# Kernel optimization log

Hardware: AMD Instinct MI355X
Metric: run time of the kernel (lower is better)

## Reference

```python
import jax, jax.numpy as jnp
from jax import lax
import numpy as np

S, D, H, DW, V, KW = 2048, 512, 512, 512, 100000, 3


def _build_gaz(rng):
    lens = rng.integers(2, 9, size=(S, KW))
    keep = (rng.random((S, KW)) < 0.5) & (np.arange(S)[:, None] + lens - 1 < S)
    word_ids = rng.integers(0, V, size=(S, KW))
    ends = [[] for _ in range(S)]
    for s in range(S):
        for j in range(KW):
            if keep[s, j]:
                ends[s + lens[s, j] - 1].append((s, j))
    Km = max(1, max(len(e) for e in ends))
    gpos = np.zeros((S, Km), np.int32)
    gslot = np.zeros((S, Km), np.int32)
    gmask = np.zeros((S, Km), bool)
    for t in range(S):
        for k, (s, j) in enumerate(ends[t]):
            gpos[t, k], gslot[t, k], gmask[t, k] = s, j, True
    return word_ids.astype(np.int32), gpos, gslot, gmask


def setup_inputs() -> dict:
    rng = np.random.default_rng(0)
    word_ids, gpos, gslot, gmask = _build_gaz(rng)
    key = jax.random.key(0)
    ks = jax.random.split(key, 12)
    f32 = jnp.float32
    inp = {
        "x": jax.random.normal(ks[0], (1, S, D), f32),
        # MultiInputLSTMCell params
        "W_ih": jax.random.normal(ks[1], (D, 3 * H), f32) / np.sqrt(D),
        "W_hh": jax.random.normal(ks[2], (H, 3 * H), f32) / np.sqrt(H),
        "b": jnp.zeros((3 * H,), f32),
        "aW_ih": jax.random.normal(ks[3], (D, H), f32) / np.sqrt(D),
        "aW_hh": jax.random.normal(ks[4], (H, H), f32) / np.sqrt(H),
        "ab": jnp.zeros((H,), f32),
        # WordLSTMCell params
        "Ww_ih": jax.random.normal(ks[5], (DW, 3 * H), f32) / np.sqrt(DW),
        "Ww_hh": jax.random.normal(ks[6], (H, 3 * H), f32) / np.sqrt(H),
        "bw": jnp.zeros((3 * H,), f32),
        # gaz word embedding table (dropout=0.0 -> identity)
        "word_emb": jax.random.normal(ks[7], (V, DW), f32) * 0.1,
        "word_ids": jnp.asarray(word_ids),
        "gather_pos": jnp.asarray(gpos),
        "gather_slot": jnp.asarray(gslot),
        "gather_mask": jnp.asarray(gmask),
    }
    return inp


def reference(x, W_ih, W_hh, b, aW_ih, aW_hh, ab, Ww_ih, Ww_hh, bw, word_emb,
              word_ids, gather_pos, gather_slot, gather_mask):
    xs = x[0]                                   # [S, D]
    WI = xs @ W_ih                              # [S, 3H] char-cell input proj
    AWI = xs @ aW_ih + ab                       # [S, H]  alpha input proj
    wemb = word_emb[word_ids]                   # [S, KW, DW] gaz embedding gather
    WWI = jnp.einsum('skd,dh->skh', wemb, Ww_ih)  # [S, KW, 3H] word-cell input proj
    gmaskf = gather_mask.astype(x.dtype)        # [S, Km]
    Hh = W_hh.shape[0]
    c_buf0 = jnp.zeros((S, word_ids.shape[1], Hh), x.dtype)  # word c^w storage by (start, slot)
    h0 = jnp.zeros((Hh,), x.dtype)
    c0 = jnp.zeros((Hh,), x.dtype)

    def step(carry, t):
        hx, cx, c_buf = carry
        # words ending at t (scattered earlier): [Km, H]
        c_in = c_buf[gather_pos[t], gather_slot[t]]
        m = gmaskf[t][:, None]
        # char cell gates
        gates = hx @ W_hh + b + WI[t]           # [3H]
        i, o, g = jnp.split(gates, 3)
        i = jax.nn.sigmoid(i); o = jax.nn.sigmoid(o); g = jnp.tanh(g)
        # exp-normalized blend over {char gate i} U {alpha_k} (masked)
        alpha = jax.nn.sigmoid(AWI[t][None, :] + c_in @ aW_hh)  # [Km, H]
        w_i = jnp.exp(i)                        # [H]
        w_a = jnp.exp(alpha) * m                # [Km, H]
        denom = w_i + w_a.sum(0)
        c_merge = (w_i * g + (w_a * c_in).sum(0)) / denom
        c_plain = (1.0 - i) * cx + i * g        # no-word branch: f = 1 - i
        has_words = gather_mask[t].any()
        c1 = jnp.where(has_words, c_merge, c_plain)
        h1 = o * jnp.tanh(c1)
        # word cells for words STARTING at t, seeded with updated (h1, c1)
        wgates = WWI[t] + (h1 @ Ww_hh + bw)[None, :]  # [KW, 3H]
        f, iw, gw = jnp.split(wgates, 3, axis=1)
        ct_w = jax.nn.sigmoid(f) * c1[None, :] + jax.nn.sigmoid(iw) * jnp.tanh(gw)
        c_buf = lax.dynamic_update_slice(c_buf, ct_w[None], (t, 0, 0))
        return (h1, c1, c_buf), (h1, c1)

    _, (hs, cs) = lax.scan(step, (h0, c0, c_buf0), jnp.arange(S))
    return hs[None], cs[None]                   # each [1, S, H]
```

## Files before the change

### kernel.cpp

```cpp
#include <hip/hip_runtime.h>

constexpr int SEQ = 2048;
constexpr int HD  = 512;
constexpr int TH3 = 1536;
constexpr int ZT  = 3072;
constexpr int KWW = 3;

constexpr int GRID = 64;
constexpr int NT   = 512;
constexpr int HB   = HD / GRID;
constexpr int SPB  = SEQ / GRID;
constexpr int MAXW = 16;

constexpr unsigned int SENT = 0xFFFFFFFFu;

constexpr size_t WS_FLAGS  = 0;
constexpr size_t WS_CNT    = 1024;
constexpr size_t WS_ZEROSZ = 2048;
constexpr size_t WS_CBUF   = 2048;
constexpr size_t WS_HFULL  = WS_CBUF + (size_t)SEQ*KWW*HD*4;
constexpr size_t WS_FFEND  = WS_HFULL + (size_t)SEQ*HD*4;
constexpr size_t WS_MHDR   = ((WS_FFEND + 255)/256)*256;
constexpr size_t WS_MROWS  = WS_MHDR + (size_t)SEQ*4;
constexpr size_t WS_WIB    = WS_MROWS + (size_t)SEQ*MAXW*4;
constexpr size_t WS_AWIB   = WS_WIB  + (size_t)SEQ*TH3*4;
constexpr size_t WS_WWIB   = WS_AWIB + (size_t)SEQ*HD*4;
constexpr size_t WS_WT     = WS_WWIB + (size_t)SEQ*KWW*TH3*4;
constexpr size_t WS_END    = WS_WT + (size_t)ZT*HD*4;

__device__ inline float bf2f(unsigned int u) {
    return __builtin_bit_cast(float, u << 16);
}
__device__ inline unsigned short f2bf(float f) {
    unsigned int u = __builtin_bit_cast(unsigned int, f);
    u += 0x7fffu + ((u >> 16) & 1u);
    return (unsigned short)(u >> 16);
}
__device__ inline float sigf(float x) { return 1.0f / (1.0f + expf(-x)); }

template <typename T>
__device__ inline T ldg_a(const T* p) {
    return __hip_atomic_load((T*)p, __ATOMIC_RELAXED, __HIP_MEMORY_SCOPE_AGENT);
}
template <typename T>
__device__ inline void stg_a(T* p, T v) {
    __hip_atomic_store(p, v, __ATOMIC_RELAXED, __HIP_MEMORY_SCOPE_AGENT);
}
__device__ inline unsigned int ldu_a(const unsigned int* p) {
    return __hip_atomic_load((unsigned int*)p, __ATOMIC_RELAXED, __HIP_MEMORY_SCOPE_AGENT);
}

__device__ inline float4 ld4e(const void* p, size_t eoff, int mode) {
    if (mode) {
        uint2 v = *(const uint2*)((const unsigned short*)p + eoff);
        return make_float4(bf2f(v.x & 0xffffu), bf2f(v.x >> 16),
                           bf2f(v.y & 0xffffu), bf2f(v.y >> 16));
    }
    return *(const float4*)((const float*)p + eoff);
}
__device__ inline float ld1e(const void* p, size_t eoff, int mode) {
    return mode ? bf2f((unsigned int)((const unsigned short*)p)[eoff])
                : ((const float*)p)[eoff];
}

constexpr int NDET = 4096;
__global__ void detect_kernel(const unsigned int* __restrict__ w, int* __restrict__ cnt) {
    int local = 0;
    for (int i = threadIdx.x; i < NDET; i += 256) {
        unsigned int e = (w[i] >> 7) & 0xffu;
        if (e >= 90u && e <= 140u) local++;
    }
    atomicAdd(cnt, local);
}

template<bool GATHER>
__global__ __launch_bounds__(256) void gemm_bias_kernel(
    const void* __restrict__ A, const void* __restrict__ B,
    const void* __restrict__ bias, const int* __restrict__ ids,
    const int* __restrict__ cnt,
    float* __restrict__ C, int M, int N, int K)
{
    const int mode = (*cnt > NDET / 2) ? 1 : 0;
    __shared__ __align__(16) float As[16][68];
    __shared__ __align__(16) float Bs[16][68];
    const int tid = threadIdx.x;
    const int ty = tid >> 4, tx = tid & 15;
    const int m0 = blockIdx.y * 64, n0 = blockIdx.x * 64;
    const int lrow = tid >> 2;
    const int kq   = (tid & 3) * 4;
    const int arow = m0 + lrow;
    const size_t abase = (GATHER ? (size_t)ids[arow] : (size_t)arow) * (size_t)K;
    const int brow = tid >> 4;
    const int bc   = (tid & 15) * 4;
    const int bcol = n0 + bc;
    float acc[4][4] = {};
    for (int k0 = 0; k0 < K; k0 += 16) {
        float4 av = ld4e(A, abase + k0 + kq, mode);
        float4 bv = ld4e(B, (size_t)(k0 + brow) * N + bcol, mode);
        As[kq + 0][lrow] = av.x;
        As[kq + 1][lrow] = av.y;
        As[kq + 2][lrow] = av.z;
        As[kq + 3][lrow] = av.w;
        Bs[brow][bc + 0] = bv.x;
        Bs[brow][bc + 1] = bv.y;
        Bs[brow][bc + 2] = bv.z;
        Bs[brow][bc + 3] = bv.w;
        __syncthreads();
        #pragma unroll
        for (int kk = 0; kk < 16; ++kk) {
            float a[4], bb[4];
            #pragma unroll
            for (int u = 0; u < 4; ++u) a[u] = As[kk][ty * 4 + u];
            #pragma unroll
            for (int v = 0; v < 4; ++v) bb[v] = Bs[kk][tx * 4 + v];
            #pragma unroll
            for (int u = 0; u < 4; ++u)
                #pragma unroll
                for (int v = 0; v < 4; ++v)
                    acc[u][v] = fmaf(a[u], bb[v], acc[u][v]);
        }
        __syncthreads();
    }
    float4 bsv = ld4e(bias, (size_t)(n0 + tx * 4), mode);
    #pragma unroll
    for (int u = 0; u < 4; ++u) {
        float4 o;
        o.x = acc[u][0] + bsv.x; o.y = acc[u][1] + bsv.y;
        o.z = acc[u][2] + bsv.z; o.w = acc[u][3] + bsv.w;
        *(float4*)(C + (size_t)(m0 + ty * 4 + u) * N + n0 + tx * 4) = o;
    }
}

__global__ __launch_bounds__(256) void transpose_cat_kernel(
    const void* __restrict__ W_hh, const void* __restrict__ Ww_hh,
    const int* __restrict__ cnt, float* __restrict__ out)
{
    const int mode = (*cnt > NDET / 2) ? 1 : 0;
    __shared__ float tile[32][33];
    const int c0 = blockIdx.x * 32;
    const int j0 = blockIdx.y * 32;
    const int tx = threadIdx.x & 31, ty = threadIdx.x >> 5;
    const void* src = (c0 < TH3) ? W_hh : Ww_hh;
    const int cc0 = (c0 < TH3) ? c0 : c0 - TH3;
    #pragma unroll
    for (int dy = 0; dy < 32; dy += 8)
        tile[ty + dy][tx] = ld1e(src, (size_t)(j0 + ty + dy) * TH3 + cc0 + tx, mode);
    __syncthreads();
    #pragma unroll
    for (int dy = 0; dy < 32; dy += 8)
        out[(size_t)(c0 + ty + dy) * HD + j0 + tx] = tile[tx][ty + dy];
}

__device__ inline void gbar(int* flags, int b, int k) {
    __atomic_signal_fence(__ATOMIC_SEQ_CST);
    __builtin_amdgcn_s_waitcnt(0);
    __syncthreads();
    if (threadIdx.x < 64) {
        if (threadIdx.x == 0) stg_a(&flags[b], k);
        for (;;) {
            int v = ldg_a(&flags[threadIdx.x]);
            if (__all(v >= k)) break;
            __builtin_amdgcn_s_sleep(1);
        }
    }
    __syncthreads();
    __atomic_signal_fence(__ATOMIC_SEQ_CST);
}

__device__ inline float wave_red(float acc) {
    #pragma unroll
    for (int m = 1; m < 64; m <<= 1) acc += __shfl_xor(acc, m, 64);
    return acc;
}

__global__ __launch_bounds__(NT, 1) void lattice_scan(
    const float* WT, const void* __restrict__ aW_hh,
    const float* __restrict__ WIb, const float* __restrict__ AWIb,
    const float* __restrict__ WWIb,
    float* hfull, float* c_buf, int* __restrict__ flags,
    const int* __restrict__ cnt,
    const int* __restrict__ gpos, const int* __restrict__ gslot,
    const unsigned char* __restrict__ gmaskb,
    int* __restrict__ meta_hdr, int* __restrict__ meta_rows,
    void* __restrict__ outp, int Km)
{
    __shared__ __align__(16) float cinS[2][MAXW][HD];
    __shared__ int mh_l[2], mr_l[2][MAXW];
    __shared__ int mfmt;

    const int b    = blockIdx.x;
    const int tid  = threadIdx.x;
    const int wid  = tid >> 6;
    const int q    = tid & 63;
    const int mode = (*cnt > NDET / 2) ? 1 : 0;
    const int hb0  = b * HB;
    const int ch   = hb0 + wid;

    float wreg[6][8];
    #pragma unroll
    for (int k = 0; k < 6; ++k)
        #pragma unroll
        for (int i = 0; i < 8; ++i)
            wreg[k][i] = WT[(size_t)(k * HD + ch) * HD + q + 64 * i];
    float aw[8];
    #pragma unroll
    for (int i = 0; i < 8; ++i)
        aw[i] = ld1e(aW_hh, (size_t)(q + 64 * i) * HD + ch, mode);

    if (tid == 0) mfmt = 0;
    __syncthreads();
    {
        int any = 0;
        int tot = SEQ * Km;
        for (int i = tid; i < tot; i += NT)
            if ((i & 3) && gmaskb[i]) any = 1;
        if (any) mfmt = 1;
    }
    __syncthreads();
    const int maskfmt = mfmt;
    const int* gmi = (const int*)gmaskb;

    if (tid < SPB) {
        int t = b * SPB + tid;
        int nv = 0;
        for (int k = 0; k < Km; ++k) {
            int mv = maskfmt ? (int)gmaskb[t * Km + k] : gmi[t * Km + k];
            if (!mv) continue;
            int p = gpos[t * Km + k], sl = gslot[t * Km + k];
            if (p < 0 || p >= t || sl < 0 || sl >= KWW) continue;
            if (nv < MAXW) { stg_a(&meta_rows[t * MAXW + nv], (p << 2) | sl); nv++; }
        }
        stg_a(&meta_hdr[t], nv);
    }
    gbar(flags, b, 1);

    if (tid == 0) mh_l[0] = ldg_a(&meta_hdr[0]);
    if (tid < MAXW) mr_l[0][tid] = ldg_a(&meta_rows[tid]);
    __syncthreads();

    float c_prev = 0.f;

    for (int t = 0; t < SEQ; ++t) {
        const int par = t & 1;
        const int nv = mh_l[par];
        bool anyl2 = false;
        for (int vi = 0; vi < nv; ++vi)
            if ((mr_l[par][vi] >> 2) == t - 1) anyl2 = true;

        float wi0 = WIb[(size_t)t * TH3 + ch];
        float wi1 = WIb[(size_t)t * TH3 + HD + ch];
        float wi2 = WIb[(size_t)t * TH3 + 2 * HD + ch];
        float wi3 = AWIb[(size_t)t * HD + ch];
        float wwf = 0.f, wwi = 0.f, wwg = 0.f;
        if (t > 0 && q < KWW) {
            const float* wr = WWIb + (size_t)((t - 1) * KWW + q) * TH3;
            wwf = wr[ch]; wwi = wr[HD + ch]; wwg = wr[2 * HD + ch];
        }
        if (t + 1 < SEQ) {
            if (tid == 0) mh_l[par ^ 1] = ldg_a(&meta_hdr[t + 1]);
            if (tid < MAXW)
                mr_l[par ^ 1][tid] = ldg_a(&meta_rows[(size_t)(t + 1) * MAXW + tid]);
        }

        {
            int g = tid >> 5, l = tid & 31;
            bool act = false;
            const unsigned int* src = nullptr;
            if (g < nv) {
                int e = mr_l[par][g], p = e >> 2, sl = e & 3;
                if (p <= t - 2)
                    { act = true; src = (const unsigned int*)(c_buf + (size_t)(p * KWW + sl) * HD); }
            }
            float v[16];
            for (;;) {
                bool ok = true;
                if (act) {
                    #pragma unroll
                    for (int i = 0; i < 16; ++i) {
                        unsigned int u = ldu_a(src + l + 32 * i);
                        v[i] = __builtin_bit_cast(float, u);
                        ok &= (u != SENT);
                    }
                }
                if (__all(ok)) break;
                __builtin_amdgcn_s_sleep(1);
            }
            if (act) {
                #pragma unroll
                for (int i = 0; i < 16; ++i) cinS[par][g][l + 32 * i] = v[i];
            }
        }

        float hv[8];
        if (t > 0) {
            const unsigned int* hrow = (const unsigned int*)(hfull + (size_t)(t - 1) * HD);
            for (;;) {
                bool ok = true;
                #pragma unroll
                for (int i = 0; i < 8; ++i) {
                    unsigned int u = ldu_a(hrow + q + 64 * i);
                    hv[i] = __builtin_bit_cast(float, u);
                    ok &= (u != SENT);
                }
                if (__all(ok)) break;
                __builtin_amdgcn_s_sleep(1);
            }
        } else {
            #pragma unroll
            for (int i = 0; i < 8; ++i) hv[i] = 0.f;
        }

        float zk[6];
        #pragma unroll
        for (int k = 0; k < 6; ++k) {
            float a = 0.f;
            #pragma unroll
            for (int i = 0; i < 8; ++i) a = fmaf(hv[i], wreg[k][i], a);
            zk[k] = wave_red(a);
        }

        if (t > 0 && q < KWW) {
            float cv = sigf(wwf + zk[3]) * c_prev
                     + sigf(wwi + zk[4]) * tanhf(wwg + zk[5]);
            stg_a(&c_buf[(size_t)((t - 1) * KWW + q) * HD + ch], cv);
        }

        if (anyl2) {
            int g = tid >> 5, l = tid & 31;
            bool act = false;
            const unsigned int* src = nullptr;
            if (g < nv) {
                int e = mr_l[par][g], p = e >> 2, sl = e & 3;
                if (p == t - 1)
                    { act = true; src = (const unsigned int*)(c_buf + (size_t)(p * KWW + sl) * HD); }
            }
            float v[16];
            for (;;) {
                bool ok = true;
                if (act) {
                    #pragma unroll
                    for (int i = 0; i < 16; ++i) {
                        unsigned int u = ldu_a(src + l + 32 * i);
                        v[i] = __builtin_bit_cast(float, u);
                        ok &= (u != SENT);
                    }
                }
                if (__all(ok)) break;
                __builtin_amdgcn_s_sleep(1);
            }
            if (act) {
                #pragma unroll
                for (int i = 0; i < 16; ++i) cinS[par][g][l + 32 * i] = v[i];
            }
        }

        __syncthreads();

        float gi = sigf(zk[0] + wi0);
        float go = sigf(zk[1] + wi1);
        float gg = tanhf(zk[2] + wi2);
        float c1;
        if (nv > 0) {
            float wiE = expf(gi);
            float num = wiE * gg, den = wiE;
            for (int vi = 0; vi < nv; ++vi) {
                float acc = 0.f;
                #pragma unroll
                for (int i = 0; i < 8; ++i)
                    acc += cinS[par][vi][q + 64 * i] * aw[i];
                acc = wave_red(acc);
                float wa = expf(sigf(wi3 + acc));
                num += wa * cinS[par][vi][ch];
                den += wa;
            }
            c1 = num / den;
        } else {
            c1 = (1.f - gi) * c_prev + gi * gg;
        }
        float h1 = go * tanhf(c1);
        c_prev = c1;
        if (q == 0) {
            stg_a(&hfull[(size_t)t * HD + ch], h1);
            if (mode) {
                unsigned short* o = (unsigned short*)outp;
                o[(size_t)t * HD + ch] = f2bf(h1);
                o[(size_t)SEQ * HD + (size_t)t * HD + ch] = f2bf(c1);
            } else {
                float* o = (float*)outp;
                o[(size_t)t * HD + ch] = h1;
                o[(size_t)SEQ * HD + (size_t)t * HD + ch] = c1;
            }
        }
    }
}

extern "C" void kernel_launch(void* const* d_in, const int* in_sizes, int n_in,
                              void* d_out, int out_size, void* d_ws, size_t ws_size,
                              hipStream_t stream) {
    const void* x     = d_in[0];
    const void* W_ih  = d_in[1];
    const void* W_hh  = d_in[2];
    const void* bb    = d_in[3];
    const void* aW_ih = d_in[4];
    const void* aW_hh = d_in[5];
    const void* ab    = d_in[6];
    const void* Ww_ih = d_in[7];
    const void* Ww_hh = d_in[8];
    const void* bw    = d_in[9];
    const void* wemb  = d_in[10];
    const int* wids  = (const int*)d_in[11];
    const int* gpos  = (const int*)d_in[12];
    const int* gslot = (const int*)d_in[13];
    const unsigned char* gmask = (const unsigned char*)d_in[14];

    int Km = in_sizes[12] / SEQ;
    if (Km > 32) Km = 32;
    if (ws_size < WS_END) return;

    char* ws = (char*)d_ws;
    int*   flags = (int*)(ws + WS_FLAGS);
    int*   cnt   = (int*)(ws + WS_CNT);
    float* c_buf = (float*)(ws + WS_CBUF);
    float* hfull = (float*)(ws + WS_HFULL);
    int*   mhdr  = (int*)(ws + WS_MHDR);
    int*   mrows = (int*)(ws + WS_MROWS);
    float* WIb   = (float*)(ws + WS_WIB);
    float* AWIb  = (float*)(ws + WS_AWIB);
    float* WWIb  = (float*)(ws + WS_WWIB);
    float* WT    = (float*)(ws + WS_WT);

    hipMemsetAsync(ws, 0, WS_ZEROSZ, stream);
    hipMemsetAsync(ws + WS_CBUF, 0xFF, WS_FFEND - WS_CBUF, stream);
    detect_kernel<<<1, 256, 0, stream>>>((const unsigned int*)W_ih, cnt);
    transpose_cat_kernel<<<dim3(ZT / 32, HD / 32), 256, 0, stream>>>(
        W_hh, Ww_hh, cnt, WT);
    gemm_bias_kernel<false><<<dim3(TH3 / 64, SEQ / 64), 256, 0, stream>>>(
        x, W_ih, bb, nullptr, cnt, WIb, SEQ, TH3, HD);
    gemm_bias_kernel<false><<<dim3(HD / 64, SEQ / 64), 256, 0, stream>>>(
        x, aW_ih, ab, nullptr, cnt, AWIb, SEQ, HD, HD);
    gemm_bias_kernel<true><<<dim3(TH3 / 64, (SEQ * KWW) / 64), 256, 0, stream>>>(
        wemb, Ww_ih, bw, wids, cnt, WWIb, SEQ * KWW, TH3, HD);
    lattice_scan<<<GRID, NT, 0, stream>>>(
        WT, aW_hh, WIb, AWIb, WWIb,
        hfull, c_buf, flags, cnt,
        gpos, gslot, gmask, mhdr, mrows, d_out, Km);
}
```

Before: 9.524 ms.

## Pin recurrent scan to one XCD with sc0 coherent polling and fewer workgroups

The scan now launches extra workgroups, elects a single XCD whose first 32 workgroups (1024 threads each, 16 channels per block) run the recurrence, and the rest exit. Keeping all participants on one XCD lets the spin-polling of h and c_buf use sc0 loads and stores that stay coherent in the shared L2, instead of agent-scope atomics that have to reach farther. A startup check confirms coherence and falls back to the atomic path if it fails. Separately, the shared-memory staging of word cell rows and the __syncthreads per step are removed, and each wave reads its c_in rows directly inside the merge loop. The risks are relying on undocumented XCD placement and coherence behaviour, spending time on the election, and getting fewer CUs for the recurrence.

```diff
diff --git a/kernel.cpp b/kernel.cpp
--- a/kernel.cpp
+++ b/kernel.cpp
@@ -6,16 +6,23 @@
 constexpr int ZT  = 3072;
 constexpr int KWW = 3;
 
-constexpr int GRID = 64;
-constexpr int NT   = 512;
-constexpr int HB   = HD / GRID;
-constexpr int SPB  = SEQ / GRID;
-constexpr int MAXW = 16;
-
-constexpr unsigned int SENT = 0xFFFFFFFFu;
+constexpr int NPART  = 32;
+constexpr int NT     = 1024;
+constexpr int CHB    = 16;
+constexpr int SPB    = SEQ / NPART;
+constexpr int MAXW   = 16;
+constexpr int NLAUNCH= 256;
+constexpr int SPIN_ESC = 1 << 16;
+
+constexpr unsigned int SENT  = 0xFFFFFFFFu;
+constexpr unsigned int MAGIC = 0x5A5A0000u;
 
 constexpr size_t WS_FLAGS  = 0;
 constexpr size_t WS_CNT    = 1024;
+constexpr size_t WS_XCNT   = 1280;
+constexpr size_t WS_ELECT  = 1312;
+constexpr size_t WS_COHF   = 1316;
+constexpr size_t WS_COHT   = 1344;
 constexpr size_t WS_ZEROSZ = 2048;
 constexpr size_t WS_CBUF   = 2048;
 constexpr size_t WS_HFULL  = WS_CBUF + (size_t)SEQ*KWW*HD*4;
@@ -48,6 +55,54 @@
 }
 __device__ inline unsigned int ldu_a(const unsigned int* p) {
     return __hip_atomic_load((unsigned int*)p, __ATOMIC_RELAXED, __HIP_MEMORY_SCOPE_AGENT);
+}
+
+__device__ inline unsigned int ld1_sc0(const unsigned int* p) {
+    unsigned int v;
+    asm volatile("global_load_dword %0, %1, off sc0\n\t"
+                 "s_waitcnt vmcnt(0)"
+                 : "=v"(v) : "v"(p) : "memory");
+    return v;
+}
+__device__ inline void st1_sc0(unsigned int* p, unsigned int v) {
+    asm volatile("global_store_dword %0, %1, off sc0" :: "v"(p), "v"(v) : "memory");
+}
+__device__ inline void row8_sc0(const unsigned int* p, unsigned int v[8]) {
+    asm volatile(
+        "global_load_dword %0, %[a], off sc0\n\t"
+        "global_load_dword %1, %[a], off offset:256 sc0\n\t"
+        "global_load_dword %2, %[a], off offset:512 sc0\n\t"
+        "global_load_dword %3, %[a], off offset:768 sc0\n\t"
+        "global_load_dword %4, %[a], off offset:1024 sc0\n\t"
+        "global_load_dword %5, %[a], off offset:1280 sc0\n\t"
+        "global_load_dword %6, %[a], off offset:1536 sc0\n\t"
+        "global_load_dword %7, %[a], off offset:1792 sc0\n\t"
+        "s_waitcnt vmcnt(0)"
+        : "=&v"(v[0]), "=&v"(v[1]), "=&v"(v[2]), "=&v"(v[3]),
+          "=&v"(v[4]), "=&v"(v[5]), "=&v"(v[6]), "=&v"(v[7])
+        : [a]"v"(p)
+        : "memory");
+}
+__device__ inline void row9_sc0(const unsigned int* p, const unsigned int* pc,
+                                unsigned int v[8], unsigned int& cv) {
+    asm volatile(
+        "global_load_dword %0, %[a], off sc0\n\t"
+        "global_load_dword %1, %[a], off offset:256 sc0\n\t"
+        "global_load_dword %2, %[a], off offset:512 sc0\n\t"
+        "global_load_dword %3, %[a], off offset:768 sc0\n\t"
+        "global_load_dword %4, %[a], off offset:1024 sc0\n\t"
+        "global_load_dword %5, %[a], off offset:1280 sc0\n\t"
+        "global_load_dword %6, %[a], off offset:1536 sc0\n\t"
+        "global_load_dword %7, %[a], off offset:1792 sc0\n\t"
+        "global_load_dword %8, %[c], off sc0\n\t"
+        "s_waitcnt vmcnt(0)"
+        : "=&v"(v[0]), "=&v"(v[1]), "=&v"(v[2]), "=&v"(v[3]),
+          "=&v"(v[4]), "=&v"(v[5]), "=&v"(v[6]), "=&v"(v[7]), "=&v"(cv)
+        : [a]"v"(p), [c]"v"(pc)
+        : "memory");
+}
+__device__ inline unsigned int get_xcc() {
+    return __builtin_amdgcn_s_getreg(20 | (0 << 6) | ((32 - 1) << 11)) & 7u;
 }
 
 __device__ inline float4 ld4e(const void* p, size_t eoff, int mode) {
@@ -158,7 +213,7 @@
     if (threadIdx.x < 64) {
         if (threadIdx.x == 0) stg_a(&flags[b], k);
         for (;;) {
-            int v = ldg_a(&flags[threadIdx.x]);
+            int v = (threadIdx.x < NPART) ? ldg_a(&flags[threadIdx.x]) : k;
             if (__all(v >= k)) break;
             __builtin_amdgcn_s_sleep(1);
         }
@@ -173,28 +228,53 @@
     return acc;
 }
 
-__global__ __launch_bounds__(NT, 1) void lattice_scan(
+__global__ __launch_bounds__(NT) void lattice_scan(
     const float* WT, const void* __restrict__ aW_hh,
     const float* __restrict__ WIb, const float* __restrict__ AWIb,
     const float* __restrict__ WWIb,
-    float* hfull, float* c_buf, int* __restrict__ flags,
+    float* hfull, float* c_buf,
+    int* flags, int* xcnt, int* elected, int* cohfail, unsigned int* coht,
     const int* __restrict__ cnt,
     const int* __restrict__ gpos, const int* __restrict__ gslot,
     const unsigned char* __restrict__ gmaskb,
     int* __restrict__ meta_hdr, int* __restrict__ meta_rows,
     void* __restrict__ outp, int Km)
 {
-    __shared__ __align__(16) float cinS[2][MAXW][HD];
-    __shared__ int mh_l[2], mr_l[2][MAXW];
-    __shared__ int mfmt;
-
-    const int b    = blockIdx.x;
+    __shared__ int sslot, sew, mfmt;
+
     const int tid  = threadIdx.x;
     const int wid  = tid >> 6;
     const int q    = tid & 63;
     const int mode = (*cnt > NDET / 2) ? 1 : 0;
-    const int hb0  = b * HB;
-    const int ch   = hb0 + wid;
+
+    const unsigned int xcd = get_xcc();
+    if (tid == 0) {
+        int slot = atomicAdd(&xcnt[xcd], 1);
+        if (slot == NPART - 1) atomicCAS(elected, 0, (int)xcd + 1);
+        sslot = slot;
+    }
+    __syncthreads();
+    const int slot = sslot;
+    if (tid == 0) {
+        long long t0 = clock64();
+        int ew;
+        for (;;) {
+            ew = ldg_a(elected);
+            if (ew != 0) break;
+            if (clock64() - t0 > 4000000ll) {
+                if (slot == 0 && ldg_a(&xcnt[xcd]) >= NPART)
+                    atomicCAS(elected, 0, (int)xcd + 1);
+                t0 = clock64();
+            }
+            __builtin_amdgcn_s_sleep(16);
+        }
+        sew = ew;
+    }
+    __syncthreads();
+    const int ew = sew;
+    if ((int)xcd != ew - 1 || slot >= NPART) return;
+    const int b  = slot;
+    const int ch = b * CHB + wid;
 
     float wreg[6][8];
     #pragma unroll
@@ -232,145 +312,140 @@
         }
         stg_a(&meta_hdr[t], nv);
     }
+    if (tid == 0) st1_sc0(&coht[b], MAGIC ^ (unsigned int)b);
     gbar(flags, b, 1);
-
-    if (tid == 0) mh_l[0] = ldg_a(&meta_hdr[0]);
-    if (tid < MAXW) mr_l[0][tid] = ldg_a(&meta_rows[tid]);
-    __syncthreads();
-
+    if (tid < NPART) {
+        unsigned int v = ld1_sc0(&coht[tid]);
+        if (v != (MAGIC ^ (unsigned int)tid)) stg_a(cohfail, 1);
+    }
+    if (tid == 0) st1_sc0(&coht[NPART + b], (MAGIC | 0xA50000u) ^ (unsigned int)b);
+    gbar(flags, b, 2);
+    if (tid < NPART) {
+        unsigned int v = ld1_sc0(&coht[NPART + tid]);
+        if (v != ((MAGIC | 0xA50000u) ^ (unsigned int)tid)) stg_a(cohfail, 1);
+    }
+    gbar(flags, b, 3);
+    const bool coh = (ldg_a(cohfail) == 0);
+
+    int nv_c = ldg_a(&meta_hdr[0]);
+    int mrow_c = (q < MAXW) ? ldg_a(&meta_rows[q]) : 0;
+
+    const unsigned int* hfu = (const unsigned int*)hfull;
+    const unsigned int* cbu = (const unsigned int*)c_buf;
     float c_prev = 0.f;
 
     for (int t = 0; t < SEQ; ++t) {
-        const int par = t & 1;
-        const int nv = mh_l[par];
-        bool anyl2 = false;
-        for (int vi = 0; vi < nv; ++vi)
-            if ((mr_l[par][vi] >> 2) == t - 1) anyl2 = true;
+        const int nv = nv_c;
+        const int mrow = mrow_c;
 
         float wi0 = WIb[(size_t)t * TH3 + ch];
         float wi1 = WIb[(size_t)t * TH3 + HD + ch];
         float wi2 = WIb[(size_t)t * TH3 + 2 * HD + ch];
         float wi3 = AWIb[(size_t)t * HD + ch];
-        float wwf = 0.f, wwi = 0.f, wwg = 0.f;
+        float wwf = 0.f, wwi2 = 0.f, wwg = 0.f;
         if (t > 0 && q < KWW) {
             const float* wr = WWIb + (size_t)((t - 1) * KWW + q) * TH3;
-            wwf = wr[ch]; wwi = wr[HD + ch]; wwg = wr[2 * HD + ch];
+            wwf = wr[ch]; wwi2 = wr[HD + ch]; wwg = wr[2 * HD + ch];
         }
         if (t + 1 < SEQ) {
-            if (tid == 0) mh_l[par ^ 1] = ldg_a(&meta_hdr[t + 1]);
-            if (tid < MAXW)
-                mr_l[par ^ 1][tid] = ldg_a(&meta_rows[(size_t)(t + 1) * MAXW + tid]);
-        }
-
-        {
-            int g = tid >> 5, l = tid & 31;
-            bool act = false;
-            const unsigned int* src = nullptr;
-            if (g < nv) {
-                int e = mr_l[par][g], p = e >> 2, sl = e & 3;
-                if (p <= t - 2)
-                    { act = true; src = (const unsigned int*)(c_buf + (size_t)(p * KWW + sl) * HD); }
-            }
-            float v[16];
-            for (;;) {
-                bool ok = true;
-                if (act) {
-                    #pragma unroll
-                    for (int i = 0; i < 16; ++i) {
-                        unsigned int u = ldu_a(src + l + 32 * i);
-                        v[i] = __builtin_bit_cast(float, u);
-                        ok &= (u != SENT);
-                    }
-                }
-                if (__all(ok)) break;
-                __builtin_amdgcn_s_sleep(1);
-            }
-            if (act) {
-                #pragma unroll
-                for (int i = 0; i < 16; ++i) cinS[par][g][l + 32 * i] = v[i];
-            }
+            nv_c = ldg_a(&meta_hdr[t + 1]);
+            mrow_c = (q < MAXW) ? ldg_a(&meta_rows[(size_t)(t + 1) * MAXW + q]) : 0;
         }
 
         float hv[8];
         if (t > 0) {
-            const unsigned int* hrow = (const unsigned int*)(hfull + (size_t)(t - 1) * HD);
-            for (;;) {
-                bool ok = true;
-                #pragma unroll
-                for (int i = 0; i < 8; ++i) {
-                    unsigned int u = ldu_a(hrow + q + 64 * i);
-                    hv[i] = __builtin_bit_cast(float, u);
-                    ok &= (u != SENT);
+            const unsigned int* hp = hfu + (size_t)(t - 1) * HD + q;
+            unsigned int v[8];
+            bool done = false;
+            if (coh) {
+                for (int spins = 0; spins < SPIN_ESC; ++spins) {
+                    row8_sc0(hp, v);
+                    bool ok = true;
+                    #pragma unroll
+                    for (int i = 0; i < 8; ++i) ok &= (v[i] != SENT);
+                    if (__all(ok)) { done = true; break; }
+                    __builtin_amdgcn_s_sleep(1);
                 }
-                if (__all(ok)) break;
-                __builtin_amdgcn_s_sleep(1);
             }
+            if (!done) {
+                for (;;) {
+                    bool ok = true;
+                    #pragma unroll
+                    for (int i = 0; i < 8; ++i) { v[i] = ldu_a(hp + 64 * i); ok &= (v[i] != SENT); }
+                    if (__all(ok)) break;
+                    __builtin_amdgcn_s_sleep(1);
+                }
+            }
+            #pragma unroll
+            for (int i = 0; i < 8; ++i) hv[i] = __builtin_bit_cast(float, v[i]);
         } else {
             #pragma unroll
             for (int i = 0; i < 8; ++i) hv[i] = 0.f;
         }
 
-        float zk[6];
+        float z3 = 0.f, z4 = 0.f, z5 = 0.f;
         #pragma unroll
-        for (int k = 0; k < 6; ++k) {
-            float a = 0.f;
-            #pragma unroll
-            for (int i = 0; i < 8; ++i) a = fmaf(hv[i], wreg[k][i], a);
-            zk[k] = wave_red(a);
-        }
-
+        for (int i = 0; i < 8; ++i) {
+            z3 = fmaf(hv[i], wreg[3][i], z3);
+            z4 = fmaf(hv[i], wreg[4][i], z4);
+            z5 = fmaf(hv[i], wreg[5][i], z5);
+        }
+        z3 = wave_red(z3); z4 = wave_red(z4); z5 = wave_red(z5);
         if (t > 0 && q < KWW) {
-            float cv = sigf(wwf + zk[3]) * c_prev
-                     + sigf(wwi + zk[4]) * tanhf(wwg + zk[5]);
-            stg_a(&c_buf[(size_t)((t - 1) * KWW + q) * HD + ch], cv);
-        }
-
-        if (anyl2) {
-            int g = tid >> 5, l = tid & 31;
-            bool act = false;
-            const unsigned int* src = nullptr;
-            if (g < nv) {
-                int e = mr_l[par][g], p = e >> 2, sl = e & 3;
-                if (p == t - 1)
-                    { act = true; src = (const unsigned int*)(c_buf + (size_t)(p * KWW + sl) * HD); }
-            }
-            float v[16];
-            for (;;) {
-                bool ok = true;
-                if (act) {
-                    #pragma unroll
-                    for (int i = 0; i < 16; ++i) {
-                        unsigned int u = ldu_a(src + l + 32 * i);
-                        v[i] = __builtin_bit_cast(float, u);
-                        ok &= (u != SENT);
-                    }
-                }
-                if (__all(ok)) break;
-                __builtin_amdgcn_s_sleep(1);
-            }
-            if (act) {
-                #pragma unroll
-                for (int i = 0; i < 16; ++i) cinS[par][g][l + 32 * i] = v[i];
-            }
-        }
-
-        __syncthreads();
-
-        float gi = sigf(zk[0] + wi0);
-        float go = sigf(zk[1] + wi1);
-        float gg = tanhf(zk[2] + wi2);
+            float cv = sigf(wwf + z3) * c_prev + sigf(wwi2 + z4) * tanhf(wwg + z5);
+            unsigned int* dst = (unsigned int*)&c_buf[(size_t)((t - 1) * KWW + q) * HD + ch];
+            if (coh) st1_sc0(dst, __builtin_bit_cast(unsigned int, cv));
+            else     stg_a((float*)dst, cv);
+        }
+
+        float z0 = 0.f, z1 = 0.f, z2 = 0.f;
+        #pragma unroll
+        for (int i = 0; i < 8; ++i) {
+            z0 = fmaf(hv[i], wreg[0][i], z0);
+            z1 = fmaf(hv[i], wreg[1][i], z1);
+            z2 = fmaf(hv[i], wreg[2][i], z2);
+        }
+        z0 = wave_red(z0); z1 = wave_red(z1); z2 = wave_red(z2);
+        float gi = sigf(z0 + wi0);
+        float go = sigf(z1 + wi1);
+        float gg = tanhf(z2 + wi2);
+
         float c1;
         if (nv > 0) {
             float wiE = expf(gi);
             float num = wiE * gg, den = wiE;
             for (int vi = 0; vi < nv; ++vi) {
+                int e = __shfl(mrow, vi);
+                const unsigned int* crow = cbu + (size_t)((e >> 2) * KWW + (e & 3)) * HD;
+                unsigned int v[8], cu;
+                bool done = false;
+                if (coh) {
+                    for (int spins = 0; spins < SPIN_ESC; ++spins) {
+                        row9_sc0(crow + q, crow + ch, v, cu);
+                        bool ok = (cu != SENT);
+                        #pragma unroll
+                        for (int i = 0; i < 8; ++i) ok &= (v[i] != SENT);
+                        if (__all(ok)) { done = true; break; }
+                        __builtin_amdgcn_s_sleep(1);
+                    }
+                }
+                if (!done) {
+                    for (;;) {
+                        cu = ldu_a(crow + ch);
+                        bool ok = (cu != SENT);
+                        #pragma unroll
+                        for (int i = 0; i < 8; ++i) { v[i] = ldu_a(crow + q + 64 * i); ok &= (v[i] != SENT); }
+                        if (__all(ok)) break;
+                        __builtin_amdgcn_s_sleep(1);
+                    }
+                }
                 float acc = 0.f;
                 #pragma unroll
                 for (int i = 0; i < 8; ++i)
-                    acc += cinS[par][vi][q + 64 * i] * aw[i];
+                    acc = fmaf(__builtin_bit_cast(float, v[i]), aw[i], acc);
                 acc = wave_red(acc);
                 float wa = expf(sigf(wi3 + acc));
-                num += wa * cinS[par][vi][ch];
+                num = fmaf(wa, __builtin_bit_cast(float, cu), num);
                 den += wa;
             }
             c1 = num / den;
@@ -379,8 +454,11 @@
         }
         float h1 = go * tanhf(c1);
         c_prev = c1;
+
         if (q == 0) {
-            stg_a(&hfull[(size_t)t * HD + ch], h1);
+            unsigned int* hd = (unsigned int*)&hfull[(size_t)t * HD + ch];
+            if (coh) st1_sc0(hd, __builtin_bit_cast(unsigned int, h1));
+            else     stg_a((float*)hd, h1);
             if (mode) {
                 unsigned short* o = (unsigned short*)outp;
                 o[(size_t)t * HD + ch] = f2bf(h1);
@@ -420,6 +498,10 @@
     char* ws = (char*)d_ws;
     int*   flags = (int*)(ws + WS_FLAGS);
     int*   cnt   = (int*)(ws + WS_CNT);
+    int*   xcnt  = (int*)(ws + WS_XCNT);
+    int*   elect = (int*)(ws + WS_ELECT);
+    int*   cohf  = (int*)(ws + WS_COHF);
+    unsigned int* coht = (unsigned int*)(ws + WS_COHT);
     float* c_buf = (float*)(ws + WS_CBUF);
     float* hfull = (float*)(ws + WS_HFULL);
     int*   mhdr  = (int*)(ws + WS_MHDR);
@@ -440,8 +522,8 @@
         x, aW_ih, ab, nullptr, cnt, AWIb, SEQ, HD, HD);
     gemm_bias_kernel<true><<<dim3(TH3 / 64, (SEQ * KWW) / 64), 256, 0, stream>>>(
         wemb, Ww_ih, bw, wids, cnt, WWIb, SEQ * KWW, TH3, HD);
-    lattice_scan<<<GRID, NT, 0, stream>>>(
+    lattice_scan<<<NLAUNCH, NT, 0, stream>>>(
         WT, aW_hh, WIb, AWIb, WWIb,
-        hfull, c_buf, flags, cnt,
+        hfull, c_buf, flags, xcnt, elect, cohf, coht, cnt,
         gpos, gslot, gmask, mhdr, mrows, d_out, Km);
 }
```

Result: slower. 20.02 ms (+110.2%).

## Load word-cell states per wave into registers, removing shared memory and block barrier

Applied to the files above, without the earlier changes.

Each wave now loads the c_buf rows it needs directly into registers. It merges the polls for h and the older word cells into one spin loop and takes metadata through shuffles, so the shared-memory staging and the per-step __syncthreads are gone. The six gate dot-products are interleaved, with their cross-lane reductions batched together. The aim is less per-timestep latency in the serial scan, paid for by more redundant global loads per wave and extra register pressure.

```diff
diff --git a/kernel.cpp b/kernel.cpp
--- a/kernel.cpp
+++ b/kernel.cpp
@@ -11,6 +11,7 @@
 constexpr int HB   = HD / GRID;
 constexpr int SPB  = SEQ / GRID;
 constexpr int MAXW = 16;
+constexpr int FMAX = 4;
 
 constexpr unsigned int SENT = 0xFFFFFFFFu;
 
@@ -48,6 +49,16 @@
 }
 __device__ inline unsigned int ldu_a(const unsigned int* p) {
     return __hip_atomic_load((unsigned int*)p, __ATOMIC_RELAXED, __HIP_MEMORY_SCOPE_AGENT);
+}
+
+__device__ inline bool ld_row8(const unsigned int* base, unsigned int ru[8]) {
+    bool ok = true;
+    #pragma unroll
+    for (int i = 0; i < 8; ++i) {
+        ru[i] = ldu_a(base + 64 * i);
+        ok &= (ru[i] != SENT);
+    }
+    return ok;
 }
 
 __device__ inline float4 ld4e(const void* p, size_t eoff, int mode) {
@@ -184,8 +195,6 @@
     int* __restrict__ meta_hdr, int* __restrict__ meta_rows,
     void* __restrict__ outp, int Km)
 {
-    __shared__ __align__(16) float cinS[2][MAXW][HD];
-    __shared__ int mh_l[2], mr_l[2][MAXW];
     __shared__ int mfmt;
 
     const int b    = blockIdx.x;
@@ -193,8 +202,9 @@
     const int wid  = tid >> 6;
     const int q    = tid & 63;
     const int mode = (*cnt > NDET / 2) ? 1 : 0;
-    const int hb0  = b * HB;
-    const int ch   = hb0 + wid;
+    const int ch   = b * HB + wid;
+    const int chHi = ch >> 6;
+    const int chLo = ch & 63;
 
     float wreg[6][8];
     #pragma unroll
@@ -234,18 +244,16 @@
     }
     gbar(flags, b, 1);
 
-    if (tid == 0) mh_l[0] = ldg_a(&meta_hdr[0]);
-    if (tid < MAXW) mr_l[0][tid] = ldg_a(&meta_rows[tid]);
-    __syncthreads();
-
+    int nv_c = meta_hdr[0];
+    int mrow_c = (q < MAXW) ? meta_rows[q] : 0;
+
+    const unsigned int* hfu = (const unsigned int*)hfull;
+    const unsigned int* cbu = (const unsigned int*)c_buf;
     float c_prev = 0.f;
 
     for (int t = 0; t < SEQ; ++t) {
-        const int par = t & 1;
-        const int nv = mh_l[par];
-        bool anyl2 = false;
-        for (int vi = 0; vi < nv; ++vi)
-            if ((mr_l[par][vi] >> 2) == t - 1) anyl2 = true;
+        const int nv = nv_c;
+        const int mrow = mrow_c;
 
         float wi0 = WIb[(size_t)t * TH3 + ch];
         float wi1 = WIb[(size_t)t * TH3 + HD + ch];
@@ -257,121 +265,127 @@
             wwf = wr[ch]; wwi = wr[HD + ch]; wwg = wr[2 * HD + ch];
         }
         if (t + 1 < SEQ) {
-            if (tid == 0) mh_l[par ^ 1] = ldg_a(&meta_hdr[t + 1]);
-            if (tid < MAXW)
-                mr_l[par ^ 1][tid] = ldg_a(&meta_rows[(size_t)(t + 1) * MAXW + tid]);
-        }
-
-        {
-            int g = tid >> 5, l = tid & 31;
-            bool act = false;
-            const unsigned int* src = nullptr;
-            if (g < nv) {
-                int e = mr_l[par][g], p = e >> 2, sl = e & 3;
-                if (p <= t - 2)
-                    { act = true; src = (const unsigned int*)(c_buf + (size_t)(p * KWW + sl) * HD); }
+            nv_c = meta_hdr[t + 1];
+            mrow_c = (q < MAXW) ? meta_rows[(size_t)(t + 1) * MAXW + q] : 0;
+        }
+
+        const unsigned int *f0 = nullptr, *f1 = nullptr, *f2 = nullptr, *f3 = nullptr;
+        const unsigned int *n0 = nullptr, *n1 = nullptr, *n2 = nullptr;
+        int nf = 0, nn = 0;
+        for (int vi = 0; vi < nv; ++vi) {
+            int e = __shfl(mrow, vi);
+            int p = e >> 2, sl = e & 3;
+            const unsigned int* base = cbu + (size_t)(p * KWW + sl) * HD + q;
+            if (p <= t - 2) {
+                if (nf == 0) f0 = base;
+                else if (nf == 1) f1 = base;
+                else if (nf == 2) f2 = base;
+                else if (nf == 3) f3 = base;
+                nf++;
+            } else {
+                if (nn == 0) n0 = base;
+                else if (nn == 1) n1 = base;
+                else n2 = base;
+                nn++;
             }
-            float v[16];
+        }
+
+        unsigned int hu[8], r0[8], r1[8], r2[8], r3[8];
+        if (t > 0 || nf > 0) {
+            const unsigned int* hp = hfu + (size_t)(t - 1) * HD + q;
             for (;;) {
                 bool ok = true;
-                if (act) {
-                    #pragma unroll
-                    for (int i = 0; i < 16; ++i) {
-                        unsigned int u = ldu_a(src + l + 32 * i);
-                        v[i] = __builtin_bit_cast(float, u);
-                        ok &= (u != SENT);
-                    }
-                }
+                if (t > 0) ok &= ld_row8(hp, hu);
+                if (f0)    ok &= ld_row8(f0, r0);
+                if (f1)    ok &= ld_row8(f1, r1);
+                if (f2)    ok &= ld_row8(f2, r2);
+                if (f3)    ok &= ld_row8(f3, r3);
                 if (__all(ok)) break;
                 __builtin_amdgcn_s_sleep(1);
             }
-            if (act) {
-                #pragma unroll
-                for (int i = 0; i < 16; ++i) cinS[par][g][l + 32 * i] = v[i];
-            }
-        }
-
+        }
         float hv[8];
         if (t > 0) {
-            const unsigned int* hrow = (const unsigned int*)(hfull + (size_t)(t - 1) * HD);
-            for (;;) {
-                bool ok = true;
-                #pragma unroll
-                for (int i = 0; i < 8; ++i) {
-                    unsigned int u = ldu_a(hrow + q + 64 * i);
-                    hv[i] = __builtin_bit_cast(float, u);
-                    ok &= (u != SENT);
-                }
-                if (__all(ok)) break;
-                __builtin_amdgcn_s_sleep(1);
-            }
+            #pragma unroll
+            for (int i = 0; i < 8; ++i) hv[i] = __builtin_bit_cast(float, hu[i]);
         } else {
             #pragma unroll
             for (int i = 0; i < 8; ++i) hv[i] = 0.f;
         }
 
-        float zk[6];
+        float z[6];
         #pragma unroll
-        for (int k = 0; k < 6; ++k) {
-            float a = 0.f;
-            #pragma unroll
-            for (int i = 0; i < 8; ++i) a = fmaf(hv[i], wreg[k][i], a);
-            zk[k] = wave_red(a);
-        }
+        for (int k = 0; k < 6; ++k) z[k] = 0.f;
+        #pragma unroll
+        for (int i = 0; i < 8; ++i)
+            #pragma unroll
+            for (int k = 0; k < 6; ++k) z[k] = fmaf(hv[i], wreg[k][i], z[k]);
+        #pragma unroll
+        for (int m = 1; m < 64; m <<= 1)
+            #pragma unroll
+            for (int k = 0; k < 6; ++k) z[k] += __shfl_xor(z[k], m, 64);
 
         if (t > 0 && q < KWW) {
-            float cv = sigf(wwf + zk[3]) * c_prev
-                     + sigf(wwi + zk[4]) * tanhf(wwg + zk[5]);
+            float cv = sigf(wwf + z[3]) * c_prev + sigf(wwi + z[4]) * tanhf(wwg + z[5]);
             stg_a(&c_buf[(size_t)((t - 1) * KWW + q) * HD + ch], cv);
         }
 
-        if (anyl2) {
-            int g = tid >> 5, l = tid & 31;
-            bool act = false;
-            const unsigned int* src = nullptr;
-            if (g < nv) {
-                int e = mr_l[par][g], p = e >> 2, sl = e & 3;
-                if (p == t - 1)
-                    { act = true; src = (const unsigned int*)(c_buf + (size_t)(p * KWW + sl) * HD); }
-            }
-            float v[16];
-            for (;;) {
-                bool ok = true;
-                if (act) {
-                    #pragma unroll
-                    for (int i = 0; i < 16; ++i) {
-                        unsigned int u = ldu_a(src + l + 32 * i);
-                        v[i] = __builtin_bit_cast(float, u);
-                        ok &= (u != SENT);
-                    }
-                }
-                if (__all(ok)) break;
-                __builtin_amdgcn_s_sleep(1);
-            }
-            if (act) {
-                #pragma unroll
-                for (int i = 0; i < 16; ++i) cinS[par][g][l + 32 * i] = v[i];
-            }
-        }
-
-        __syncthreads();
-
-        float gi = sigf(zk[0] + wi0);
-        float go = sigf(zk[1] + wi1);
-        float gg = tanhf(zk[2] + wi2);
+        float gi = sigf(z[0] + wi0);
+        float go = sigf(z[1] + wi1);
+        float gg = tanhf(z[2] + wi2);
         float c1;
         if (nv > 0) {
             float wiE = expf(gi);
             float num = wiE * gg, den = wiE;
-            for (int vi = 0; vi < nv; ++vi) {
+            auto alpha_acc = [&](const unsigned int ru[8]) {
                 float acc = 0.f;
                 #pragma unroll
                 for (int i = 0; i < 8; ++i)
-                    acc += cinS[par][vi][q + 64 * i] * aw[i];
+                    acc = fmaf(__builtin_bit_cast(float, ru[i]), aw[i], acc);
                 acc = wave_red(acc);
+                float cv_ = 0.f;
+                #pragma unroll
+                for (int i = 0; i < 8; ++i)
+                    if (i == chHi) cv_ = __builtin_bit_cast(float, ru[i]);
+                cv_ = __shfl(cv_, chLo);
                 float wa = expf(sigf(wi3 + acc));
-                num += wa * cinS[par][vi][ch];
+                num = fmaf(wa, cv_, num);
                 den += wa;
+            };
+            if (f0) alpha_acc(r0);
+            if (f1) alpha_acc(r1);
+            if (f2) alpha_acc(r2);
+            if (f3) alpha_acc(r3);
+            if (nf > FMAX) {
+                int fseen = 0;
+                for (int vi = 0; vi < nv; ++vi) {
+                    int e = __shfl(mrow, vi);
+                    int p = e >> 2, sl = e & 3;
+                    if (p > t - 2) continue;
+                    fseen++;
+                    if (fseen <= FMAX) continue;
+                    const unsigned int* base = cbu + (size_t)(p * KWW + sl) * HD + q;
+                    unsigned int ru[8];
+                    for (;;) {
+                        if (__all(ld_row8(base, ru))) break;
+                        __builtin_amdgcn_s_sleep(1);
+                    }
+                    alpha_acc(ru);
+                }
+            }
+            if (nn > 0) {
+                unsigned int a0[8], a1[8], a2[8];
+                for (;;) {
+                    bool ok = true;
+                    if (n0) ok &= ld_row8(n0, a0);
+                    if (n1) ok &= ld_row8(n1, a1);
+                    if (n2) ok &= ld_row8(n2, a2);
+                    if (__all(ok)) break;
+                    __builtin_amdgcn_s_sleep(1);
+                }
+                if (n0) alpha_acc(a0);
+                if (n1) alpha_acc(a1);
+                if (n2) alpha_acc(a2);
             }
             c1 = num / den;
         } else {
```

After: 8.334 ms. 1.14x faster.
